# Kernel optimization log

Hardware: AMD Instinct MI355X
Metric: run time of the kernel (lower is better)

Reference implementation:

```python
import jax, jax.numpy as jnp
import numpy as np

BETA = 1.0  # write blending coefficient (beta in original module)


def ste(x):
    # Binarize with straight-through estimator: forward (x>0.5), backward identity.
    b = (x > 0.5).astype(x.dtype)
    return x + jax.lax.stop_gradient(b - x)


def setup_inputs() -> dict:
    key = jax.random.key(0)
    k0, k1, k2 = jax.random.split(key, 3)
    B, H, W, HID = 8, 512, 512, 64
    f0 = jax.random.uniform(k0, (B, 1, H, W), dtype=jnp.float32)
    W1 = jax.random.normal(k1, (9, HID), dtype=jnp.float32) * (1.0 / np.sqrt(9.0))
    b1 = jnp.zeros((HID,), dtype=jnp.float32)
    W2 = jax.random.normal(k2, (HID, 1), dtype=jnp.float32) * (1.0 / np.sqrt(HID))
    b2 = jnp.zeros((1,), dtype=jnp.float32)
    return {"f0": f0, "W1": W1, "b1": b1, "W2": W2, "b2": b2, "T": 16}


def reference(f0, W1, b1, W2, b2, T):
    B, _, H, Wd = f0.shape

    def step(f, _):
        f_read = ste(f)                                            # (B,1,H,W) binarized read
        pad = jnp.pad(f_read, ((0, 0), (0, 0), (1, 1), (1, 1)), mode="wrap")
        # 3x3 neighborhoods, row-major top-left -> bottom-right: (B,H,W,9)
        neigh = jnp.stack(
            [pad[:, 0, i:i + H, j:j + Wd] for i in range(3) for j in range(3)],
            axis=-1,
        )
        h = jax.nn.relu(jnp.einsum("bhwn,nk->bhwk", neigh, W1) + b1)
        logits = (jnp.einsum("bhwk,ko->bhwo", h, W2) + b2)[..., 0]  # (B,H,W)
        w_bits = ste(jax.nn.sigmoid(logits))[:, None]               # (B,1,H,W)
        f_new = (1.0 - BETA) * f + BETA * w_bits
        return f_new, f_new

    _, rest = jax.lax.scan(step, f0, None, length=T - 1)
    fields = jnp.concatenate([f0[None], rest], axis=0)  # (T,B,1,H,W)
    return fields
```

## Files before the change

### kernel.cpp

```cpp
#include <hip/hip_runtime.h>

#define HH 512
#define WW 512
#define WPR 16
#define RO 16
#define HALO 15
#define ROWS (RO + 2 * HALO)
#define OW 8
#define TW 10

__global__ __launch_bounds__(256) void init_field(const float* __restrict__ f0,
                                                  float* __restrict__ out,
                                                  unsigned long long* __restrict__ field) {
    int c = blockIdx.x * 256 + threadIdx.x;
    float v = f0[c];
    out[c] = v;
    unsigned long long m = __ballot(v > 0.5f);
    if ((threadIdx.x & 63) == 0) field[c >> 6] = m;
}

__global__ __launch_bounds__(512) void mega(const unsigned int* __restrict__ field,
                                            const float* __restrict__ W1,
                                            const float* __restrict__ b1,
                                            const float* __restrict__ W2,
                                            const float* __restrict__ b2,
                                            int hid, float* __restrict__ out,
                                            int n, int T) {
    __shared__ unsigned int rule[512];
    __shared__ unsigned int lut[256];
    __shared__ unsigned int bufA[ROWS * TW];
    __shared__ unsigned int bufB[ROWS * TW];

    const int tid = threadIdx.x;
    const int cg = blockIdx.x & 1;
    const int rg = (blockIdx.x >> 1) & 31;
    const int b  = blockIdx.x >> 6;
    const int r0 = rg * RO;
    const int q0 = cg * OW;
    const int c0 = cg * (OW * 32);

    {
        int p = tid;
        float logit = b2[0];
        for (int k = 0; k < hid; ++k) {
            float a = b1[k];
#pragma unroll
            for (int nn = 0; nn < 9; ++nn)
                if (p & (1 << nn)) a += W1[nn * hid + k];
            logit += fmaxf(a, 0.0f) * W2[k];
        }
        rule[p] = (logit > 0.0f) ? 1u : 0u;
    }
    __syncthreads();

    if (tid < 256) {
        unsigned int wv = 0;
#pragma unroll
        for (int k = 0; k < 16; ++k) {
            unsigned int e = (unsigned int)tid * 16u + k;
            unsigned int u = e & 15u, m = (e >> 4) & 15u, d = (e >> 8) & 15u;
            unsigned int i0 = (u & 7u) | ((m & 7u) << 3) | ((d & 7u) << 6);
            unsigned int i1 = (u >> 1) | ((m >> 1) << 3) | ((d >> 1) << 6);
            wv |= (rule[i0] | (rule[i1] << 1)) << (2 * k);
        }
        lut[tid] = wv;
    }

    {
        const unsigned int* F = field + b * (HH * WPR);
        for (int i = tid; i < ROWS * TW; i += 512) {
            int l = i / TW, tw = i - l * TW;
            int g  = (r0 - HALO + l) & (HH - 1);
            int gw = (q0 - 1 + tw) & (WPR - 1);
            bufA[i] = F[g * WPR + gw];
        }
    }
    __syncthreads();

    unsigned int* oldb = bufA;
    unsigned int* newb = bufB;
    float* outb = out + (size_t)b * (HH * WW);

    for (int t = 1; t < T; ++t) {
        const int hi = ROWS - t;
        const int lq = tid / TW;
        const int w  = tid - lq * TW;
        const int l  = t + lq;
        if (l < hi) {
            const unsigned int* Ru = oldb + (l - 1) * TW;
            const unsigned int* Rm = oldb + l * TW;
            const unsigned int* Rd = oldb + (l + 1) * TW;
            const int wl = (w == 0) ? 0 : w - 1;
            const int wn = (w == TW - 1) ? TW - 1 : w + 1;
            unsigned long long eu = ((((unsigned long long)Ru[wn] << 32) | Ru[w]) << 1) | (Ru[wl] >> 31);
            unsigned long long em = ((((unsigned long long)Rm[wn] << 32) | Rm[w]) << 1) | (Rm[wl] >> 31);
            unsigned long long ed = ((((unsigned long long)Rd[wn] << 32) | Rd[w]) << 1) | (Rd[wl] >> 31);
            unsigned int ow = 0;
#pragma unroll
            for (int j = 0; j < 16; ++j) {
                unsigned int idx = (unsigned int)((eu >> (2 * j)) & 15ull)
                                 | ((unsigned int)((em >> (2 * j)) & 15ull) << 4)
                                 | ((unsigned int)((ed >> (2 * j)) & 15ull) << 8);
                ow |= ((lut[idx >> 4] >> ((idx & 15u) * 2)) & 3u) << (2 * j);
            }
            newb[l * TW + w] = ow;
        }
        __syncthreads();

        float* outt = outb + (size_t)t * n;
#pragma unroll
        for (int rep = 0; rep < 2; ++rep) {
            int cell = (rep * 512 + tid) * 4;
            int lr  = cell >> 8;
            int col = cell & 255;
            unsigned int wv = newb[(HALO + lr) * TW + 1 + (col >> 5)];
            unsigned int nib = (wv >> (col & 31)) & 15u;
            float4 v;
            v.x = (float)(nib & 1u);
            v.y = (float)((nib >> 1) & 1u);
            v.z = (float)((nib >> 2) & 1u);
            v.w = (float)(nib >> 3);
            *(float4*)(outt + (size_t)(r0 + lr) * WW + c0 + col) = v;
        }
        unsigned int* tmp = oldb; oldb = newb; newb = tmp;
    }
}

extern "C" void kernel_launch(void* const* d_in, const int* in_sizes, int n_in,
                              void* d_out, int out_size, void* d_ws, size_t ws_size,
                              hipStream_t stream) {
    const float* f0 = (const float*)d_in[0];
    const float* W1 = (const float*)d_in[1];
    const float* b1 = (const float*)d_in[2];
    const float* W2 = (const float*)d_in[3];
    const float* b2 = (const float*)d_in[4];
    float* out = (float*)d_out;

    const int n = in_sizes[0];
    const int hid = in_sizes[2];
    const int T = out_size / n;
    const int B = n / (HH * WW);

    unsigned long long* fld = (unsigned long long*)d_ws;

    init_field<<<n / 256, 256, 0, stream>>>(f0, out, fld);
    mega<<<B * (HH / RO) * 2, 512, 0, stream>>>((const unsigned int*)fld,
                                                W1, b1, W2, b2, hid, out, n, T);
}
```

Measured before the change: 66.69 us.

## Split temporal blocking into two launches and replicate LUT per bank

New measurement: 111.3 us. 66.9% more time.

```diff
diff --git a/kernel.cpp b/kernel.cpp
--- a/kernel.cpp
+++ b/kernel.cpp
@@ -4,8 +4,6 @@
 #define WW 512
 #define WPR 16
 #define RO 16
-#define HALO 15
-#define ROWS (RO + 2 * HALO)
 #define OW 8
 #define TW 10
 
@@ -19,15 +17,19 @@
     if ((threadIdx.x & 63) == 0) field[c >> 6] = m;
 }
 
+template <int NSTEP, bool EMITF>
 __global__ __launch_bounds__(512) void mega(const unsigned int* __restrict__ field,
+                                            unsigned int* __restrict__ fieldOut,
                                             const float* __restrict__ W1,
                                             const float* __restrict__ b1,
                                             const float* __restrict__ W2,
                                             const float* __restrict__ b2,
                                             int hid, float* __restrict__ out,
-                                            int n, int T) {
+                                            int n, int t0) {
+    constexpr int ROWS = RO + 2 * NSTEP;
     __shared__ unsigned int rule[512];
-    __shared__ unsigned int lut[256];
+    __shared__ unsigned int lutp[256];
+    __shared__ unsigned int lutr[256 * 32];
     __shared__ unsigned int bufA[ROWS * TW];
     __shared__ unsigned int bufB[ROWS * TW];
 
@@ -38,6 +40,7 @@
     const int r0 = rg * RO;
     const int q0 = cg * OW;
     const int c0 = cg * (OW * 32);
+    const unsigned int bank = (unsigned int)(tid & 31);
 
     {
         int p = tid;
@@ -63,14 +66,16 @@
             unsigned int i1 = (u >> 1) | ((m >> 1) << 3) | ((d >> 1) << 6);
             wv |= (rule[i0] | (rule[i1] << 1)) << (2 * k);
         }
-        lut[tid] = wv;
+        lutp[tid] = wv;
     }
+    __syncthreads();
 
+    for (int i = tid; i < 256 * 32; i += 512) lutr[i] = lutp[i >> 5];
     {
         const unsigned int* F = field + b * (HH * WPR);
         for (int i = tid; i < ROWS * TW; i += 512) {
             int l = i / TW, tw = i - l * TW;
-            int g  = (r0 - HALO + l) & (HH - 1);
+            int g  = (r0 - NSTEP + l) & (HH - 1);
             int gw = (q0 - 1 + tw) & (WPR - 1);
             bufA[i] = F[g * WPR + gw];
         }
@@ -81,11 +86,11 @@
     unsigned int* newb = bufB;
     float* outb = out + (size_t)b * (HH * WW);
 
-    for (int t = 1; t < T; ++t) {
-        const int hi = ROWS - t;
+    for (int s = 1; s <= NSTEP; ++s) {
+        const int hi = ROWS - s;
         const int lq = tid / TW;
         const int w  = tid - lq * TW;
-        const int l  = t + lq;
+        const int l  = s + lq;
         if (l < hi) {
             const unsigned int* Ru = oldb + (l - 1) * TW;
             const unsigned int* Rm = oldb + l * TW;
@@ -101,19 +106,20 @@
                 unsigned int idx = (unsigned int)((eu >> (2 * j)) & 15ull)
                                  | ((unsigned int)((em >> (2 * j)) & 15ull) << 4)
                                  | ((unsigned int)((ed >> (2 * j)) & 15ull) << 8);
-                ow |= ((lut[idx >> 4] >> ((idx & 15u) * 2)) & 3u) << (2 * j);
+                unsigned int entry = lutr[((idx >> 4) << 5) | bank];
+                ow |= ((entry >> ((idx & 15u) * 2)) & 3u) << (2 * j);
             }
             newb[l * TW + w] = ow;
         }
         __syncthreads();
 
-        float* outt = outb + (size_t)t * n;
+        float* outt = outb + (size_t)(t0 + s) * n;
 #pragma unroll
         for (int rep = 0; rep < 2; ++rep) {
             int cell = (rep * 512 + tid) * 4;
             int lr  = cell >> 8;
             int col = cell & 255;
-            unsigned int wv = newb[(HALO + lr) * TW + 1 + (col >> 5)];
+            unsigned int wv = newb[(NSTEP + lr) * TW + 1 + (col >> 5)];
             unsigned int nib = (wv >> (col & 31)) & 15u;
             float4 v;
             v.x = (float)(nib & 1u);
@@ -121,6 +127,11 @@
             v.z = (float)((nib >> 2) & 1u);
             v.w = (float)(nib >> 3);
             *(float4*)(outt + (size_t)(r0 + lr) * WW + c0 + col) = v;
+        }
+        if (EMITF && s == NSTEP && tid < RO * OW) {
+            int row = tid >> 3, w2 = tid & 7;
+            fieldOut[b * (HH * WPR) + (r0 + row) * WPR + q0 + w2] =
+                newb[(NSTEP + row) * TW + 1 + w2];
         }
         unsigned int* tmp = oldb; oldb = newb; newb = tmp;
     }
@@ -138,12 +149,15 @@
 
     const int n = in_sizes[0];
     const int hid = in_sizes[2];
-    const int T = out_size / n;
     const int B = n / (HH * WW);
 
-    unsigned long long* fld = (unsigned long long*)d_ws;
+    char* ws = (char*)d_ws;
+    unsigned long long* fldA = (unsigned long long*)ws;
+    unsigned int* fldB = (unsigned int*)(ws + (size_t)(n / 8));
 
-    init_field<<<n / 256, 256, 0, stream>>>(f0, out, fld);
-    mega<<<B * (HH / RO) * 2, 512, 0, stream>>>((const unsigned int*)fld,
-                                                W1, b1, W2, b2, hid, out, n, T);
+    init_field<<<n / 256, 256, 0, stream>>>(f0, out, fldA);
+    mega<8, true><<<B * (HH / RO) * 2, 512, 0, stream>>>(
+        (const unsigned int*)fldA, fldB, W1, b1, W2, b2, hid, out, n, 0);
+    mega<7, false><<<B * (HH / RO) * 2, 512, 0, stream>>>(
+        (const unsigned int*)fldB, nullptr, W1, b1, W2, b2, hid, out, n, 8);
 }
```

## Fuse field binarization into mega kernel and defer output writes to end

Applied to the files above, without the earlier changes.

After: 87.81 us. +31.7%, slower.

```diff
diff --git a/kernel.cpp b/kernel.cpp
--- a/kernel.cpp
+++ b/kernel.cpp
@@ -4,32 +4,24 @@
 #define WW 512
 #define WPR 16
 #define RO 16
-#define HALO 15
-#define ROWS (RO + 2 * HALO)
+#define NSTEP 15
+#define ROWS (RO + 2 * NSTEP)
 #define OW 8
 #define TW 10
+#define TCOLS (TW * 32)
 
-__global__ __launch_bounds__(256) void init_field(const float* __restrict__ f0,
-                                                  float* __restrict__ out,
-                                                  unsigned long long* __restrict__ field) {
-    int c = blockIdx.x * 256 + threadIdx.x;
-    float v = f0[c];
-    out[c] = v;
-    unsigned long long m = __ballot(v > 0.5f);
-    if ((threadIdx.x & 63) == 0) field[c >> 6] = m;
-}
-
-__global__ __launch_bounds__(512) void mega(const unsigned int* __restrict__ field,
+__global__ __launch_bounds__(512) void mega(const float* __restrict__ f0,
                                             const float* __restrict__ W1,
                                             const float* __restrict__ b1,
                                             const float* __restrict__ W2,
                                             const float* __restrict__ b2,
                                             int hid, float* __restrict__ out,
-                                            int n, int T) {
+                                            int n) {
     __shared__ unsigned int rule[512];
-    __shared__ unsigned int lut[256];
+    __shared__ unsigned int lutp[256];
     __shared__ unsigned int bufA[ROWS * TW];
     __shared__ unsigned int bufB[ROWS * TW];
+    __shared__ unsigned int obits[NSTEP * RO * OW];
 
     const int tid = threadIdx.x;
     const int cg = blockIdx.x & 1;
@@ -38,6 +30,7 @@
     const int r0 = rg * RO;
     const int q0 = cg * OW;
     const int c0 = cg * (OW * 32);
+    (void)q0;
 
     {
         int p = tid;
@@ -63,29 +56,35 @@
             unsigned int i1 = (u >> 1) | ((m >> 1) << 3) | ((d >> 1) << 6);
             wv |= (rule[i0] | (rule[i1] << 1)) << (2 * k);
         }
-        lut[tid] = wv;
+        lutp[tid] = wv;
     }
 
     {
-        const unsigned int* F = field + b * (HH * WPR);
-        for (int i = tid; i < ROWS * TW; i += 512) {
-            int l = i / TW, tw = i - l * TW;
-            int g  = (r0 - HALO + l) & (HH - 1);
-            int gw = (q0 - 1 + tw) & (WPR - 1);
-            bufA[i] = F[g * WPR + gw];
+        const float* f0b = f0 + (size_t)b * (HH * WW);
+        float* out0 = out + (size_t)b * (HH * WW);
+        for (int i = tid; i < ROWS * TCOLS; i += 512) {
+            int l = i / TCOLS, c = i - l * TCOLS;
+            int gr = (r0 - NSTEP + l) & (HH - 1);
+            int gc = (c0 - 32 + c) & (WW - 1);
+            float v = f0b[(size_t)gr * WW + gc];
+            unsigned long long m = __ballot(v > 0.5f);
+            int lane = tid & 63;
+            if (lane == 0)  bufA[l * TW + (c >> 5)] = (unsigned int)m;
+            if (lane == 32) bufA[l * TW + (c >> 5)] = (unsigned int)(m >> 32);
+            if (l >= NSTEP && l < NSTEP + RO && c >= 32 && c < 32 + 256)
+                out0[(size_t)gr * WW + gc] = v;
         }
     }
     __syncthreads();
 
     unsigned int* oldb = bufA;
     unsigned int* newb = bufB;
-    float* outb = out + (size_t)b * (HH * WW);
 
-    for (int t = 1; t < T; ++t) {
-        const int hi = ROWS - t;
+    for (int s = 1; s <= NSTEP; ++s) {
+        const int hi = ROWS - s;
         const int lq = tid / TW;
         const int w  = tid - lq * TW;
-        const int l  = t + lq;
+        const int l  = s + lq;
         if (l < hi) {
             const unsigned int* Ru = oldb + (l - 1) * TW;
             const unsigned int* Rm = oldb + l * TW;
@@ -101,28 +100,34 @@
                 unsigned int idx = (unsigned int)((eu >> (2 * j)) & 15ull)
                                  | ((unsigned int)((em >> (2 * j)) & 15ull) << 4)
                                  | ((unsigned int)((ed >> (2 * j)) & 15ull) << 8);
-                ow |= ((lut[idx >> 4] >> ((idx & 15u) * 2)) & 3u) << (2 * j);
+                ow |= ((lutp[idx >> 4] >> ((idx & 15u) * 2)) & 3u) << (2 * j);
             }
             newb[l * TW + w] = ow;
+            if (l >= NSTEP && l < NSTEP + RO && w >= 1 && w <= OW)
+                obits[(s - 1) * (RO * OW) + (l - NSTEP) * OW + (w - 1)] = ow;
         }
         __syncthreads();
+        unsigned int* tmp = oldb; oldb = newb; newb = tmp;
+    }
 
-        float* outt = outb + (size_t)t * n;
-#pragma unroll
-        for (int rep = 0; rep < 2; ++rep) {
-            int cell = (rep * 512 + tid) * 4;
+    {
+        float* outb = out + (size_t)b * (HH * WW);
+#pragma unroll 2
+        for (int rep = 0; rep < 2 * NSTEP; ++rep) {
+            int idx4 = (rep * 512 + tid) * 4;
+            int s   = idx4 >> 12;
+            int cell = idx4 & 4095;
             int lr  = cell >> 8;
             int col = cell & 255;
-            unsigned int wv = newb[(HALO + lr) * TW + 1 + (col >> 5)];
+            unsigned int wv = obits[s * (RO * OW) + lr * OW + (col >> 5)];
             unsigned int nib = (wv >> (col & 31)) & 15u;
             float4 v;
             v.x = (float)(nib & 1u);
             v.y = (float)((nib >> 1) & 1u);
             v.z = (float)((nib >> 2) & 1u);
             v.w = (float)(nib >> 3);
-            *(float4*)(outt + (size_t)(r0 + lr) * WW + c0 + col) = v;
+            *(float4*)(outb + (size_t)(s + 1) * n + (size_t)(r0 + lr) * WW + c0 + col) = v;
         }
-        unsigned int* tmp = oldb; oldb = newb; newb = tmp;
     }
 }
 
@@ -138,12 +143,7 @@
 
     const int n = in_sizes[0];
     const int hid = in_sizes[2];
-    const int T = out_size / n;
     const int B = n / (HH * WW);
 
-    unsigned long long* fld = (unsigned long long*)d_ws;
-
-    init_field<<<n / 256, 256, 0, stream>>>(f0, out, fld);
-    mega<<<B * (HH / RO) * 2, 512, 0, stream>>>((const unsigned int*)fld,
-                                                W1, b1, W2, b2, hid, out, n, T);
+    mega<<<B * (HH / RO) * 2, 512, 0, stream>>>(f0, W1, b1, W2, b2, hid, out, n);
 }
```
